# Optimization experiments

Hardware: AMD Instinct MI355X
Metric: run time of the kernel (lower is better)

The kernel has to match this reference:

```python
import jax, jax.numpy as jnp
import numpy as np

N_NODES = 100000


def _gcn_conv(x, W, b, row, col, norm, n):
    # PyG GCNConv: h = x @ W, then symmetric-normalized scatter-add, then bias
    h = x @ W                          # [N, out]
    msg = h[col] * norm[:, None]       # gather at source nodes, scale per-edge
    out = jax.ops.segment_sum(msg, row, num_segments=n)  # scatter-add to dest
    return out + b


def setup_inputs() -> dict:
    key = jax.random.key(0)
    k1, k2, k3, k4, k5, k6 = jax.random.split(key, 6)
    F_in, H, C = 128, 128, 64
    E = 1600000
    x = jax.random.normal(k1, (N_NODES, F_in), dtype=jnp.float32)
    edge_index = jax.random.randint(k2, (2, E), 0, N_NODES, dtype=jnp.int64)
    s1 = 1.0 / np.sqrt(F_in)
    s2 = 1.0 / np.sqrt(H)
    W1 = jax.random.uniform(k3, (F_in, H), jnp.float32, -s1, s1)
    b1 = jax.random.uniform(k4, (H,), jnp.float32, -s1, s1)
    W2 = jax.random.uniform(k5, (H, C), jnp.float32, -s2, s2)
    b2 = jax.random.uniform(k6, (C,), jnp.float32, -s2, s2)
    return {"x": x, "edge_index": edge_index, "W1": W1, "b1": b1, "W2": W2, "b2": b2}


def reference(x, edge_index, W1, b1, W2, b2):
    n = x.shape[0]
    # add self-loops (GCNConv default)
    loops = jnp.arange(n, dtype=edge_index.dtype)
    row = jnp.concatenate([edge_index[0], loops])  # destination
    col = jnp.concatenate([edge_index[1], loops])  # source
    # symmetric normalization deg^{-1/2}[row] * deg^{-1/2}[col]
    deg = jax.ops.segment_sum(jnp.ones_like(row, dtype=x.dtype), row, num_segments=n)
    dinv = jnp.where(deg > 0, jax.lax.rsqrt(deg), 0.0)
    norm = dinv[row] * dinv[col]       # [E+N]
    h = jax.nn.relu(_gcn_conv(x, W1, b1, row, col, norm, n))
    # dropout is identity in eval mode
    out = _gcn_conv(h, W2, b2, row, col, norm, n)
    return jax.nn.log_softmax(out, axis=1)
```

## Files before the change

### kernel.cpp

```cpp
#include <hip/hip_runtime.h>
#include <hip/hip_fp16.h>
#include <cstdint>
#include <cstddef>

#define TPB 256
#define NWIN 8
#define CAP 64

using half8 = __attribute__((ext_vector_type(8))) _Float16;
using f32x4 = __attribute__((ext_vector_type(4))) float;

__global__ void k_setup(const void* __restrict__ ei, int E, int N,
                        const float* __restrict__ W1, const float* __restrict__ W2,
                        _Float16* __restrict__ wf1, _Float16* __restrict__ wf2,
                        int* __restrict__ cnt, int2* __restrict__ pairs, int nCnt) {
    int b = blockIdx.x;
    if (b < 16) {
        int i = b * TPB + threadIdx.x;
        int k  = i >> 5;
        int n0 = (i & 31) * 4;
        float4 w = ((const float4*)W1)[i];
        int ct = n0 >> 4, kb = k >> 5;
        int lane0 = ((k >> 3) & 3) * 16 + (n0 & 15);
        int j = k & 7;
        int base = ((ct * 4 + kb) * 64 + lane0) * 8 + j;
        wf1[base]      = (_Float16)w.x;
        wf1[base + 8]  = (_Float16)w.y;
        wf1[base + 16] = (_Float16)w.z;
        wf1[base + 24] = (_Float16)w.w;
    } else if (b < 24) {
        int i = (b - 16) * TPB + threadIdx.x;
        int k  = i >> 4;
        int n0 = (i & 15) * 4;
        float4 w = ((const float4*)W2)[i];
        int ct = n0 >> 4, kb = k >> 5;
        int lane0 = ((k >> 3) & 3) * 16 + (n0 & 15);
        int j = k & 7;
        int base = ((ct * 4 + kb) * 64 + lane0) * 8 + j;
        wf2[base]      = (_Float16)w.x;
        wf2[base + 8]  = (_Float16)w.y;
        wf2[base + 16] = (_Float16)w.z;
        wf2[base + 24] = (_Float16)w.w;
    } else if (b < 24 + nCnt) {
        int i = (b - 24) * TPB + threadIdx.x;
        if (i < N) cnt[i] = 0;
    } else {
        __shared__ int bad;
        if (threadIdx.x == 0) bad = 0;
        __syncthreads();
        if (threadIdx.x < 256) {
            long long v = ((const long long*)ei)[threadIdx.x];
            if (v < 0 || v >= (long long)N) bad = 1;
        }
        __syncthreads();
        int is64 = !bad;
        int base = ((b - 24 - nCnt) * TPB + threadIdx.x) * 4;
        if (base >= E) return;
        if (is64) {
            const long long* e64 = (const long long*)ei;
#pragma unroll
            for (int k = 0; k < 4; ++k)
                if (base + k < E)
                    pairs[base + k] = make_int2((int)e64[base + k],
                                                (int)e64[(long long)E + base + k]);
        } else {
            const int* e32 = (const int*)ei;
#pragma unroll
            for (int k = 0; k < 4; ++k)
                if (base + k < E)
                    pairs[base + k] = make_int2(e32[base + k], e32[E + base + k]);
        }
    }
}

__global__ __launch_bounds__(256)
void k_mega(const int2* __restrict__ pairs, int E, int winRows, int N,
            int* __restrict__ cnt, int* __restrict__ slots,
            const float* __restrict__ x, const half8* __restrict__ wf1,
            __half* __restrict__ xw1, int nFill, int nGemm) {
    __shared__ __align__(16) _Float16 Of[4][16 * 136];

    if ((int)blockIdx.x < nFill) {
        const int w = blockIdx.x & (NWIN - 1);
        const int lo = w * winRows, hi = lo + winRows;
        const int nChunks = (E + 1023) >> 10;
        const int stride = nFill / NWIN;
        for (int chunk = blockIdx.x / NWIN; chunk < nChunks; chunk += stride) {
            int base = (chunk << 10) + threadIdx.x * 4;
            if (base >= E) continue;
            int2 p[4];
            if (base + 3 < E) {
                const int4* p4 = (const int4*)(pairs + base);
                int4 u0 = p4[0], u1 = p4[1];
                p[0] = make_int2(u0.x, u0.y); p[1] = make_int2(u0.z, u0.w);
                p[2] = make_int2(u1.x, u1.y); p[3] = make_int2(u1.z, u1.w);
            } else {
#pragma unroll
                for (int k = 0; k < 4; ++k)
                    p[k] = (base + k < E) ? pairs[base + k] : make_int2(-1, -1);
            }
            int pos[4];
#pragma unroll
            for (int k = 0; k < 4; ++k) {
                bool in = (p[k].x >= lo && p[k].x < hi);
                pos[k] = in ? atomicAdd(&cnt[p[k].x], 1) : -1;
            }
#pragma unroll
            for (int k = 0; k < 4; ++k)
                if (pos[k] >= 0 && pos[k] < CAP)
                    slots[(size_t)p[k].x * CAP + pos[k]] = p[k].y;
        }
    } else {
        const int gb = blockIdx.x - nFill;
        const int wave = threadIdx.x >> 6, lane = threadIdx.x & 63;
        const int m = lane & 15, quad = lane >> 4;
        const int nRowTiles = (N + 15) >> 4;

        for (int rt = gb * 4 + wave; rt < nRowTiles; rt += nGemm * 4) {
            const int row0 = rt * 16;
            const int arow = row0 + m;
            const bool rvalid = arow < N;
            const float* xrow = x + (size_t)(rvalid ? arow : 0) * 128;

            f32x4 acc[8];
#pragma unroll
            for (int ct = 0; ct < 8; ++ct) acc[ct] = (f32x4){0.f, 0.f, 0.f, 0.f};

#pragma unroll
            for (int kb = 0; kb < 4; ++kb) {
                const float4* ap = (const float4*)(xrow + kb * 32 + quad * 8);
                float4 a0 = ap[0], a1 = ap[1];
                half8 a;
                a[0] = (_Float16)a0.x; a[1] = (_Float16)a0.y;
                a[2] = (_Float16)a0.z; a[3] = (_Float16)a0.w;
                a[4] = (_Float16)a1.x; a[5] = (_Float16)a1.y;
                a[6] = (_Float16)a1.z; a[7] = (_Float16)a1.w;
#pragma unroll
                for (int ct = 0; ct < 8; ++ct) {
                    half8 b = wf1[(ct * 4 + kb) * 64 + lane];
                    acc[ct] = __builtin_amdgcn_mfma_f32_16x16x32_f16(a, b, acc[ct], 0, 0, 0);
                }
            }

            _Float16* myO = &Of[wave][0];
#pragma unroll
            for (int ct = 0; ct < 8; ++ct)
#pragma unroll
                for (int r = 0; r < 4; ++r)
                    myO[(quad * 4 + r) * 136 + ct * 16 + m] = (_Float16)acc[ct][r];
            int vr = N - row0; if (vr > 16) vr = 16;
            float4* dst = (float4*)(xw1 + (size_t)row0 * 128);
            for (int i = lane; i < vr * 16; i += 64) {
                int r = i >> 4, q = i & 15;
                dst[r * 16 + q] = *(const float4*)&myO[r * 136 + q * 8];
            }
        }
    }
}

__global__ __launch_bounds__(256)
void k_g1g2(const __half* __restrict__ xw1, const int* __restrict__ cnt,
            const int* __restrict__ slots, const float* __restrict__ bias,
            const half8* __restrict__ wf2, __half* __restrict__ xw2, int N) {
    __shared__ __align__(16) _Float16 Ht[16 * 136];
    __shared__ __align__(16) _Float16 Of[16 * 72];

    const int row0 = blockIdx.x * 16;
    const int local = threadIdx.x >> 4;
    const int lane16 = threadIdx.x & 15;
    const int node = row0 + local;

    {
        union { __half2 h2[4]; float4 f; } u;
        if (node < N) {
            int cn = cnt[node];
            int len = cn > CAP ? CAP : cn;
            float dvn = rsqrtf((float)cn + 1.0f);
            const int* sl = slots + (size_t)node * CAP;
            float acc[8];
            {
                float4 raw = *(const float4*)(xw1 + (size_t)node * 128 + lane16 * 8);
                const __half2* hp = (const __half2*)&raw;
#pragma unroll
                for (int k = 0; k < 4; ++k) {
                    float2 f = __half22float2(hp[k]);
                    acc[2 * k] = dvn * f.x; acc[2 * k + 1] = dvn * f.y;
                }
            }
            int j = 0;
            for (; j + 3 < len; j += 4) {
                int4 cc = *(const int4*)(sl + j);
                float dv0 = rsqrtf((float)cnt[cc.x] + 1.0f);
                float dv1 = rsqrtf((float)cnt[cc.y] + 1.0f);
                float dv2 = rsqrtf((float)cnt[cc.z] + 1.0f);
                float dv3 = rsqrtf((float)cnt[cc.w] + 1.0f);
                float4 raw0 = *(const float4*)(xw1 + (size_t)cc.x * 128 + lane16 * 8);
                float4 raw1 = *(const float4*)(xw1 + (size_t)cc.y * 128 + lane16 * 8);
                float4 raw2 = *(const float4*)(xw1 + (size_t)cc.z * 128 + lane16 * 8);
                float4 raw3 = *(const float4*)(xw1 + (size_t)cc.w * 128 + lane16 * 8);
                const __half2* h0 = (const __half2*)&raw0;
                const __half2* h1 = (const __half2*)&raw1;
                const __half2* h2 = (const __half2*)&raw2;
                const __half2* h3 = (const __half2*)&raw3;
#pragma unroll
                for (int k = 0; k < 4; ++k) {
                    float2 f0 = __half22float2(h0[k]);
                    float2 f1 = __half22float2(h1[k]);
                    float2 f2 = __half22float2(h2[k]);
                    float2 f3 = __half22float2(h3[k]);
                    acc[2 * k]     = fmaf(dv0, f0.x, fmaf(dv1, f1.x,
                                     fmaf(dv2, f2.x, fmaf(dv3, f3.x, acc[2 * k]))));
                    acc[2 * k + 1] = fmaf(dv0, f0.y, fmaf(dv1, f1.y,
                                     fmaf(dv2, f2.y, fmaf(dv3, f3.y, acc[2 * k + 1]))));
                }
            }
            for (; j < len; ++j) {
                int c = sl[j];
                float dv = rsqrtf((float)cnt[c] + 1.0f);
                float4 raw = *(const float4*)(xw1 + (size_t)c * 128 + lane16 * 8);
                const __half2* hp = (const __half2*)&raw;
#pragma unroll
                for (int k = 0; k < 4; ++k) {
                    float2 f = __half22float2(hp[k]);
                    acc[2 * k]     = fmaf(dv, f.x, acc[2 * k]);
                    acc[2 * k + 1] = fmaf(dv, f.y, acc[2 * k + 1]);
                }
            }
            float4 b01 = ((const float4*)bias)[lane16 * 2];
            float4 b23 = ((const float4*)bias)[lane16 * 2 + 1];
            float v[8];
            v[0] = b01.x + dvn * acc[0]; v[1] = b01.y + dvn * acc[1];
            v[2] = b01.z + dvn * acc[2]; v[3] = b01.w + dvn * acc[3];
            v[4] = b23.x + dvn * acc[4]; v[5] = b23.y + dvn * acc[5];
            v[6] = b23.z + dvn * acc[6]; v[7] = b23.w + dvn * acc[7];
#pragma unroll
            for (int k = 0; k < 4; ++k)
                u.h2[k] = __floats2half2_rn(fmaxf(v[2 * k], 0.f), fmaxf(v[2 * k + 1], 0.f));
        } else {
            u.f = make_float4(0.f, 0.f, 0.f, 0.f);
        }
        *(float4*)(Ht + local * 136 + lane16 * 8) = u.f;
    }
    __syncthreads();

    {
        const int wave = threadIdx.x >> 6, lane = threadIdx.x & 63;
        const int m = lane & 15, quad = lane >> 4;
        f32x4 acc = (f32x4){0.f, 0.f, 0.f, 0.f};
#pragma unroll
        for (int kb = 0; kb < 4; ++kb) {
            half8 a = *(const half8*)(Ht + m * 136 + kb * 32 + quad * 8);
            half8 b = wf2[(wave * 4 + kb) * 64 + lane];
            acc = __builtin_amdgcn_mfma_f32_16x16x32_f16(a, b, acc, 0, 0, 0);
        }
#pragma unroll
        for (int r = 0; r < 4; ++r)
            Of[(quad * 4 + r) * 72 + wave * 16 + m] = (_Float16)acc[r];
    }
    __syncthreads();
    {
        int vr = N - row0; if (vr > 16) vr = 16;
        float4* dst = (float4*)(xw2 + (size_t)row0 * 64);
        for (int i = threadIdx.x; i < vr * 8; i += TPB) {
            int r = i >> 3, q = i & 7;
            dst[r * 8 + q] = *(const float4*)&Of[r * 72 + q * 8];
        }
    }
}

__global__ void k_gather2_lsm(const __half* __restrict__ xws, const int* __restrict__ cnt,
                              const int* __restrict__ slots,
                              const float* __restrict__ bias, float* __restrict__ out, int N) {
    long long t = (long long)blockIdx.x * TPB + threadIdx.x;
    int node = (int)(t >> 4);
    int lane = (int)(t & 15);
    if (node >= N) return;
    int cn = cnt[node];
    int len = cn > CAP ? CAP : cn;
    float dvn = rsqrtf((float)cn + 1.0f);
    const int* sl = slots + (size_t)node * CAP;
    float a0, a1, a2, a3;
    {
        float2 raw = *(const float2*)(xws + (size_t)node * 64 + lane * 4);
        const __half2* hp = (const __half2*)&raw;
        float2 f0 = __half22float2(hp[0]), f1 = __half22float2(hp[1]);
        a0 = dvn * f0.x; a1 = dvn * f0.y; a2 = dvn * f1.x; a3 = dvn * f1.y;
    }
    int j = 0;
    for (; j + 3 < len; j += 4) {
        int4 cc = *(const int4*)(sl + j);
        float dv0 = rsqrtf((float)cnt[cc.x] + 1.0f);
        float dv1 = rsqrtf((float)cnt[cc.y] + 1.0f);
        float dv2 = rsqrtf((float)cnt[cc.z] + 1.0f);
        float dv3 = rsqrtf((float)cnt[cc.w] + 1.0f);
        float2 raw0 = *(const float2*)(xws + (size_t)cc.x * 64 + lane * 4);
        float2 raw1 = *(const float2*)(xws + (size_t)cc.y * 64 + lane * 4);
        float2 raw2 = *(const float2*)(xws + (size_t)cc.z * 64 + lane * 4);
        float2 raw3 = *(const float2*)(xws + (size_t)cc.w * 64 + lane * 4);
        const __half2* h0 = (const __half2*)&raw0;
        const __half2* h1 = (const __half2*)&raw1;
        const __half2* h2 = (const __half2*)&raw2;
        const __half2* h3 = (const __half2*)&raw3;
        float2 f00 = __half22float2(h0[0]), f01 = __half22float2(h0[1]);
        float2 f10 = __half22float2(h1[0]), f11 = __half22float2(h1[1]);
        float2 f20 = __half22float2(h2[0]), f21 = __half22float2(h2[1]);
        float2 f30 = __half22float2(h3[0]), f31 = __half22float2(h3[1]);
        a0 = fmaf(dv0, f00.x, fmaf(dv1, f10.x, fmaf(dv2, f20.x, fmaf(dv3, f30.x, a0))));
        a1 = fmaf(dv0, f00.y, fmaf(dv1, f10.y, fmaf(dv2, f20.y, fmaf(dv3, f30.y, a1))));
        a2 = fmaf(dv0, f01.x, fmaf(dv1, f11.x, fmaf(dv2, f21.x, fmaf(dv3, f31.x, a2))));
        a3 = fmaf(dv0, f01.y, fmaf(dv1, f11.y, fmaf(dv2, f21.y, fmaf(dv3, f31.y, a3))));
    }
    for (; j < len; ++j) {
        int c = sl[j];
        float dv = rsqrtf((float)cnt[c] + 1.0f);
        float2 raw = *(const float2*)(xws + (size_t)c * 64 + lane * 4);
        const __half2* hp = (const __half2*)&raw;
        float2 f0 = __half22float2(hp[0]), f1 = __half22float2(hp[1]);
        a0 = fmaf(dv, f0.x, a0); a1 = fmaf(dv, f0.y, a1);
        a2 = fmaf(dv, f1.x, a2); a3 = fmaf(dv, f1.y, a3);
    }
    float4 bb = ((const float4*)bias)[lane];
    float v0 = bb.x + dvn * a0, v1 = bb.y + dvn * a1;
    float v2 = bb.z + dvn * a2, v3 = bb.w + dvn * a3;

    float m = fmaxf(fmaxf(v0, v1), fmaxf(v2, v3));
#pragma unroll
    for (int off = 1; off < 16; off <<= 1) m = fmaxf(m, __shfl_xor(m, off));
    float s = expf(v0 - m) + expf(v1 - m) + expf(v2 - m) + expf(v3 - m);
#pragma unroll
    for (int off = 1; off < 16; off <<= 1) s += __shfl_xor(s, off);
    float ls = m + logf(s);
    ((float4*)(out + (size_t)node * 64))[lane] =
        make_float4(v0 - ls, v1 - ls, v2 - ls, v3 - ls);
}

extern "C" void kernel_launch(void* const* d_in, const int* in_sizes, int n_in,
                              void* d_out, int out_size, void* d_ws, size_t ws_size,
                              hipStream_t stream) {
    const float* x  = (const float*)d_in[0];
    const void*  ei = d_in[1];
    const float* W1 = (const float*)d_in[2];
    const float* b1 = (const float*)d_in[3];
    const float* W2 = (const float*)d_in[4];
    const float* b2 = (const float*)d_in[5];
    float* out = (float*)d_out;

    const int N = in_sizes[0] / 128;
    const int E = in_sizes[1] / 2;

    char* base = (char*)d_ws;
    size_t off = 0;
    auto alloc = [&](size_t bytes) { char* p = base + off; off = (off + bytes + 255) & ~(size_t)255; return p; };
    int*      cnt   = (int*)alloc((size_t)N * sizeof(int));
    _Float16* wf1   = (_Float16*)alloc(128 * 128 * sizeof(_Float16));
    _Float16* wf2   = (_Float16*)alloc(128 * 64 * sizeof(_Float16));
    int2*     pairs = (int2*)alloc((size_t)E * sizeof(int2));
    int*      slots = (int*)alloc((size_t)N * CAP * sizeof(int));
    __half*   xw1   = (__half*)alloc((size_t)N * 128 * sizeof(__half));
    __half*   xw2   = (__half*)alloc((size_t)N * 64 * sizeof(__half));
    (void)ws_size;

    const int winRows = (N + NWIN - 1) / NWIN;
    const int nFill = 1024, nGemm = 512;
    const int nodeTiles = (N + 15) / 16;
    const int nCnt = (N + TPB - 1) / TPB;
    const int nDec = (E + TPB * 4 - 1) / (TPB * 4);

    k_setup<<<24 + nCnt + nDec, TPB, 0, stream>>>(ei, E, N, W1, W2, wf1, wf2,
                                                  cnt, pairs, nCnt);

    k_mega<<<nFill + nGemm, TPB, 0, stream>>>(pairs, E, winRows, N, cnt, slots,
                                              x, (const half8*)wf1, xw1, nFill, nGemm);

    k_g1g2<<<nodeTiles, TPB, 0, stream>>>(xw1, cnt, slots, b1, (const half8*)wf2, xw2, N);

    {
        long long t = (long long)N * 16;
        k_gather2_lsm<<<(int)((t + TPB - 1) / TPB), TPB, 0, stream>>>(xw2, cnt, slots, b2, out, N);
    }
}
```

Baseline: 287.3 us.

## Gather neighbors in source-node windows to improve cache locality in aggregation

Both gather kernels now walk each node's neighbor list NWIN times, each pass touching only neighbors whose source index falls in one row window. The aim is that blocks running concurrently hit the same slice of the feature table and so reuse L2/MALL. In exchange each neighbor list is re-read eight times, and the four-wide unrolled gather becomes branchy per-neighbor loads with less memory-level parallelism.

```diff
diff --git a/kernel.cpp b/kernel.cpp
--- a/kernel.cpp
+++ b/kernel.cpp
@@ -161,7 +161,8 @@
 __global__ __launch_bounds__(256)
 void k_g1g2(const __half* __restrict__ xw1, const int* __restrict__ cnt,
             const int* __restrict__ slots, const float* __restrict__ bias,
-            const half8* __restrict__ wf2, __half* __restrict__ xw2, int N) {
+            const half8* __restrict__ wf2, __half* __restrict__ xw2, int N,
+            int winRows) {
     __shared__ __align__(16) _Float16 Ht[16 * 136];
     __shared__ __align__(16) _Float16 Of[16 * 72];
 
@@ -187,43 +188,40 @@
                     acc[2 * k] = dvn * f.x; acc[2 * k + 1] = dvn * f.y;
                 }
             }
-            int j = 0;
-            for (; j + 3 < len; j += 4) {
-                int4 cc = *(const int4*)(sl + j);
-                float dv0 = rsqrtf((float)cnt[cc.x] + 1.0f);
-                float dv1 = rsqrtf((float)cnt[cc.y] + 1.0f);
-                float dv2 = rsqrtf((float)cnt[cc.z] + 1.0f);
-                float dv3 = rsqrtf((float)cnt[cc.w] + 1.0f);
-                float4 raw0 = *(const float4*)(xw1 + (size_t)cc.x * 128 + lane16 * 8);
-                float4 raw1 = *(const float4*)(xw1 + (size_t)cc.y * 128 + lane16 * 8);
-                float4 raw2 = *(const float4*)(xw1 + (size_t)cc.z * 128 + lane16 * 8);
-                float4 raw3 = *(const float4*)(xw1 + (size_t)cc.w * 128 + lane16 * 8);
-                const __half2* h0 = (const __half2*)&raw0;
-                const __half2* h1 = (const __half2*)&raw1;
-                const __half2* h2 = (const __half2*)&raw2;
-                const __half2* h3 = (const __half2*)&raw3;
-#pragma unroll
-                for (int k = 0; k < 4; ++k) {
-                    float2 f0 = __half22float2(h0[k]);
-                    float2 f1 = __half22float2(h1[k]);
-                    float2 f2 = __half22float2(h2[k]);
-                    float2 f3 = __half22float2(h3[k]);
-                    acc[2 * k]     = fmaf(dv0, f0.x, fmaf(dv1, f1.x,
-                                     fmaf(dv2, f2.x, fmaf(dv3, f3.x, acc[2 * k]))));
-                    acc[2 * k + 1] = fmaf(dv0, f0.y, fmaf(dv1, f1.y,
-                                     fmaf(dv2, f2.y, fmaf(dv3, f3.y, acc[2 * k + 1]))));
-                }
-            }
-            for (; j < len; ++j) {
-                int c = sl[j];
-                float dv = rsqrtf((float)cnt[c] + 1.0f);
-                float4 raw = *(const float4*)(xw1 + (size_t)c * 128 + lane16 * 8);
-                const __half2* hp = (const __half2*)&raw;
-#pragma unroll
-                for (int k = 0; k < 4; ++k) {
-                    float2 f = __half22float2(hp[k]);
-                    acc[2 * k]     = fmaf(dv, f.x, acc[2 * k]);
-                    acc[2 * k + 1] = fmaf(dv, f.y, acc[2 * k + 1]);
+            for (int win = 0; win < NWIN; ++win) {
+                const int lo = win * winRows, hi = lo + winRows;
+                int j = 0;
+                for (; j + 3 < len; j += 4) {
+                    int4 cc = *(const int4*)(sl + j);
+#pragma unroll
+                    for (int k = 0; k < 4; ++k) {
+                        int c = (k == 0) ? cc.x : (k == 1) ? cc.y : (k == 2) ? cc.z : cc.w;
+                        if (c >= lo && c < hi) {
+                            float dv = rsqrtf((float)cnt[c] + 1.0f);
+                            float4 raw = *(const float4*)(xw1 + (size_t)c * 128 + lane16 * 8);
+                            const __half2* hp = (const __half2*)&raw;
+#pragma unroll
+                            for (int q = 0; q < 4; ++q) {
+                                float2 f = __half22float2(hp[q]);
+                                acc[2 * q]     = fmaf(dv, f.x, acc[2 * q]);
+                                acc[2 * q + 1] = fmaf(dv, f.y, acc[2 * q + 1]);
+                            }
+                        }
+                    }
+                }
+                for (; j < len; ++j) {
+                    int c = sl[j];
+                    if (c >= lo && c < hi) {
+                        float dv = rsqrtf((float)cnt[c] + 1.0f);
+                        float4 raw = *(const float4*)(xw1 + (size_t)c * 128 + lane16 * 8);
+                        const __half2* hp = (const __half2*)&raw;
+#pragma unroll
+                        for (int q = 0; q < 4; ++q) {
+                            float2 f = __half22float2(hp[q]);
+                            acc[2 * q]     = fmaf(dv, f.x, acc[2 * q]);
+                            acc[2 * q + 1] = fmaf(dv, f.y, acc[2 * q + 1]);
+                        }
+                    }
                 }
             }
             float4 b01 = ((const float4*)bias)[lane16 * 2];
@@ -270,7 +268,8 @@
 
 __global__ void k_gather2_lsm(const __half* __restrict__ xws, const int* __restrict__ cnt,
                               const int* __restrict__ slots,
-                              const float* __restrict__ bias, float* __restrict__ out, int N) {
+                              const float* __restrict__ bias, float* __restrict__ out,
+                              int N, int winRows) {
     long long t = (long long)blockIdx.x * TPB + threadIdx.x;
     int node = (int)(t >> 4);
     int lane = (int)(t & 15);
@@ -286,38 +285,35 @@
         float2 f0 = __half22float2(hp[0]), f1 = __half22float2(hp[1]);
         a0 = dvn * f0.x; a1 = dvn * f0.y; a2 = dvn * f1.x; a3 = dvn * f1.y;
     }
-    int j = 0;
-    for (; j + 3 < len; j += 4) {
-        int4 cc = *(const int4*)(sl + j);
-        float dv0 = rsqrtf((float)cnt[cc.x] + 1.0f);
-        float dv1 = rsqrtf((float)cnt[cc.y] + 1.0f);
-        float dv2 = rsqrtf((float)cnt[cc.z] + 1.0f);
-        float dv3 = rsqrtf((float)cnt[cc.w] + 1.0f);
-        float2 raw0 = *(const float2*)(xws + (size_t)cc.x * 64 + lane * 4);
-        float2 raw1 = *(const float2*)(xws + (size_t)cc.y * 64 + lane * 4);
-        float2 raw2 = *(const float2*)(xws + (size_t)cc.z * 64 + lane * 4);
-        float2 raw3 = *(const float2*)(xws + (size_t)cc.w * 64 + lane * 4);
-        const __half2* h0 = (const __half2*)&raw0;
-        const __half2* h1 = (const __half2*)&raw1;
-        const __half2* h2 = (const __half2*)&raw2;
-        const __half2* h3 = (const __half2*)&raw3;
-        float2 f00 = __half22float2(h0[0]), f01 = __half22float2(h0[1]);
-        float2 f10 = __half22float2(h1[0]), f11 = __half22float2(h1[1]);
-        float2 f20 = __half22float2(h2[0]), f21 = __half22float2(h2[1]);
-        float2 f30 = __half22float2(h3[0]), f31 = __half22float2(h3[1]);
-        a0 = fmaf(dv0, f00.x, fmaf(dv1, f10.x, fmaf(dv2, f20.x, fmaf(dv3, f30.x, a0))));
-        a1 = fmaf(dv0, f00.y, fmaf(dv1, f10.y, fmaf(dv2, f20.y, fmaf(dv3, f30.y, a1))));
-        a2 = fmaf(dv0, f01.x, fmaf(dv1, f11.x, fmaf(dv2, f21.x, fmaf(dv3, f31.x, a2))));
-        a3 = fmaf(dv0, f01.y, fmaf(dv1, f11.y, fmaf(dv2, f21.y, fmaf(dv3, f31.y, a3))));
-    }
-    for (; j < len; ++j) {
-        int c = sl[j];
-        float dv = rsqrtf((float)cnt[c] + 1.0f);
-        float2 raw = *(const float2*)(xws + (size_t)c * 64 + lane * 4);
-        const __half2* hp = (const __half2*)&raw;
-        float2 f0 = __half22float2(hp[0]), f1 = __half22float2(hp[1]);
-        a0 = fmaf(dv, f0.x, a0); a1 = fmaf(dv, f0.y, a1);
-        a2 = fmaf(dv, f1.x, a2); a3 = fmaf(dv, f1.y, a3);
+    for (int win = 0; win < NWIN; ++win) {
+        const int lo = win * winRows, hi = lo + winRows;
+        int j = 0;
+        for (; j + 3 < len; j += 4) {
+            int4 cc = *(const int4*)(sl + j);
+#pragma unroll
+            for (int k = 0; k < 4; ++k) {
+                int c = (k == 0) ? cc.x : (k == 1) ? cc.y : (k == 2) ? cc.z : cc.w;
+                if (c >= lo && c < hi) {
+                    float dv = rsqrtf((float)cnt[c] + 1.0f);
+                    float2 raw = *(const float2*)(xws + (size_t)c * 64 + lane * 4);
+                    const __half2* hp = (const __half2*)&raw;
+                    float2 f0 = __half22float2(hp[0]), f1 = __half22float2(hp[1]);
+                    a0 = fmaf(dv, f0.x, a0); a1 = fmaf(dv, f0.y, a1);
+                    a2 = fmaf(dv, f1.x, a2); a3 = fmaf(dv, f1.y, a3);
+                }
+            }
+        }
+        for (; j < len; ++j) {
+            int c = sl[j];
+            if (c >= lo && c < hi) {
+                float dv = rsqrtf((float)cnt[c] + 1.0f);
+                float2 raw = *(const float2*)(xws + (size_t)c * 64 + lane * 4);
+                const __half2* hp = (const __half2*)&raw;
+                float2 f0 = __half22float2(hp[0]), f1 = __half22float2(hp[1]);
+                a0 = fmaf(dv, f0.x, a0); a1 = fmaf(dv, f0.y, a1);
+                a2 = fmaf(dv, f1.x, a2); a3 = fmaf(dv, f1.y, a3);
+            }
+        }
     }
     float4 bb = ((const float4*)bias)[lane];
     float v0 = bb.x + dvn * a0, v1 = bb.y + dvn * a1;
@@ -372,10 +368,12 @@
     k_mega<<<nFill + nGemm, TPB, 0, stream>>>(pairs, E, winRows, N, cnt, slots,
                                               x, (const half8*)wf1, xw1, nFill, nGemm);
 
-    k_g1g2<<<nodeTiles, TPB, 0, stream>>>(xw1, cnt, slots, b1, (const half8*)wf2, xw2, N);
+    k_g1g2<<<nodeTiles, TPB, 0, stream>>>(xw1, cnt, slots, b1, (const half8*)wf2,
+                                          xw2, N, winRows);
 
     {
         long long t = (long long)N * 16;
-        k_gather2_lsm<<<(int)((t + TPB - 1) / TPB), TPB, 0, stream>>>(xw2, cnt, slots, b2, out, N);
-    }
-}
+        k_gather2_lsm<<<(int)((t + TPB - 1) / TPB), TPB, 0, stream>>>(xw2, cnt, slots,
+                                                                      b2, out, N, winRows);
+    }
+}
```

Result: slower. 541.5 us (+88.5%).
